# Kernel tuning notes

Measured on AMD Instinct MI355X. Metric: run time of the kernel, lower is better.

Reference implementation:

```python
import jax, jax.numpy as jnp
import numpy as np

N_NODES = 100000
N_EDGES = 3200000
D_IN = 128
D_OUT = 128


def setup_inputs() -> dict:
    key = jax.random.key(0)
    k1, k2, k3, k4, k5, k6 = jax.random.split(key, 6)
    x = jax.random.normal(k1, (N_NODES, D_IN), dtype=jnp.float32)
    stdv = 1.0 / np.sqrt(D_OUT)
    weight = jax.random.normal(k2, (D_IN, D_OUT), dtype=jnp.float32) * stdv
    bias = jax.random.normal(k3, (D_OUT,), dtype=jnp.float32) * stdv
    edge_row = jax.random.randint(k4, (N_EDGES,), 0, N_NODES, dtype=jnp.int32)
    edge_col = jax.random.randint(k5, (N_EDGES,), 0, N_NODES, dtype=jnp.int32)
    edge_vals = jax.random.uniform(k6, (N_EDGES,), dtype=jnp.float32)
    return {"x": x, "weight": weight, "bias": bias,
            "edge_row": edge_row, "edge_col": edge_col, "edge_vals": edge_vals}


def reference(x, weight, bias, edge_row, edge_col, edge_vals):
    # support = input @ W   (dense GEMM, [N, D_out])
    support = x @ weight
    # spmm = adj @ support  with adj in COO form: out[r] += v * support[c]
    messages = edge_vals[:, None] * support[edge_col]  # [E, D_out]
    agg = jax.ops.segment_sum(messages, edge_row, num_segments=N_NODES)
    return agg + bias
```

## Files before the change

kernel.cpp:

```cpp
#include <hip/hip_runtime.h>

#define D 128
#define GEMM_ROWS 32
#define NB_MAX 1600
#define T_TILES 256

__device__ __forceinline__ unsigned bf16_rne(float f) {
    const unsigned u = __float_as_uint(f);
    return (u + 0x7FFFu + ((u >> 16) & 1u)) >> 16;
}
__device__ __forceinline__ float bf_lo(unsigned u) { return __uint_as_float(u << 16); }
__device__ __forceinline__ float bf_hi(unsigned u) { return __uint_as_float(u & 0xFFFF0000u); }

__global__ __launch_bounds__(256) void gcn_gemm(const float* __restrict__ x,
                                                const float* __restrict__ w,
                                                unsigned* __restrict__ support,
                                                int n_nodes) {
    __shared__ float w_lds[D][D];
    __shared__ float x_lds[GEMM_ROWS][D];
    const int t = threadIdx.x;

    {
        const float4* w4 = (const float4*)w;
        float4* wl = (float4*)&w_lds[0][0];
#pragma unroll
        for (int i = 0; i < 16; ++i) wl[t + 256 * i] = w4[t + 256 * i];
    }
    const long row_base = (long)blockIdx.x * GEMM_ROWS;
    {
        const float4* x4 = (const float4*)(x + row_base * D);
        float4* xl = (float4*)&x_lds[0][0];
#pragma unroll
        for (int i = 0; i < 4; ++i) xl[t + 256 * i] = x4[t + 256 * i];
    }
    __syncthreads();

    const int c = t & 31;
    const int rg = t >> 5;

    float4 acc[4];
#pragma unroll
    for (int j = 0; j < 4; ++j) acc[j] = make_float4(0.f, 0.f, 0.f, 0.f);

#pragma unroll 4
    for (int k = 0; k < D; ++k) {
        const float4 wv = ((const float4*)&w_lds[k][0])[c];
#pragma unroll
        for (int j = 0; j < 4; ++j) {
            const float xv = x_lds[rg * 4 + j][k];
            acc[j].x += xv * wv.x;
            acc[j].y += xv * wv.y;
            acc[j].z += xv * wv.z;
            acc[j].w += xv * wv.w;
        }
    }

#pragma unroll
    for (int j = 0; j < 4; ++j) {
        const long r = row_base + rg * 4 + j;
        uint2 pk;
        pk.x = bf16_rne(acc[j].x) | (bf16_rne(acc[j].y) << 16);
        pk.y = bf16_rne(acc[j].z) | (bf16_rne(acc[j].w) << 16);
        ((uint2*)support)[r * 32 + c] = pk;
    }
}

__global__ __launch_bounds__(1024) void gcn_tile_hist(const int* __restrict__ erow,
                                                      int* __restrict__ M,
                                                      int n_edges, int tile_sz, int nb) {
    __shared__ int h[NB_MAX];
    const int t = threadIdx.x;
    for (int i = t; i < nb; i += 1024) h[i] = 0;
    __syncthreads();
    const int beg = blockIdx.x * tile_sz;
    const int end = min(beg + tile_sz, n_edges);
    for (int e = beg + t; e < end; e += 1024)
        atomicAdd(&h[erow[e] >> 6], 1);
    __syncthreads();
    int* Mrow = M + (long)blockIdx.x * nb;
    for (int i = t; i < nb; i += 1024) Mrow[i] = h[i];
}

__global__ __launch_bounds__(256) void gcn_tile_offsets(int* __restrict__ M,
                                                        int* __restrict__ totals,
                                                        int nb) {
    const int cb = blockIdx.x * 256 + threadIdx.x;
    if (cb >= nb) return;
    int running = 0;
#pragma unroll 8
    for (int tt = 0; tt < T_TILES; ++tt) {
        int* p = M + (long)tt * nb + cb;
        const int c = *p;
        *p = running;
        running += c;
    }
    totals[cb] = running;
}

__global__ __launch_bounds__(1024) void gcn_scan_base(const int* __restrict__ totals,
                                                      int* __restrict__ base, int nb) {
    __shared__ int sdata[1024];
    const int t = threadIdx.x;
    const int chunk = (nb + 1023) >> 10;
    const int beg = min(t * chunk, nb);
    const int end = min(beg + chunk, nb);

    int sum = 0;
    for (int i = beg; i < end; ++i) sum += totals[i];
    sdata[t] = sum;
    __syncthreads();
    for (int off = 1; off < 1024; off <<= 1) {
        const int v = (t >= off) ? sdata[t - off] : 0;
        __syncthreads();
        sdata[t] += v;
        __syncthreads();
    }
    int running = sdata[t] - sum;
    if (t == 1023) base[nb] = sdata[1023];
    for (int i = beg; i < end; ++i) {
        const int c = totals[i];
        base[i] = running;
        running += c;
    }
}

__global__ __launch_bounds__(1024) void gcn_split(const int* __restrict__ erow,
                                                  const int* __restrict__ ecol,
                                                  const float* __restrict__ eval,
                                                  const int* __restrict__ M,
                                                  const int* __restrict__ base,
                                                  int2* __restrict__ tmp,
                                                  int n_edges, int tile_sz, int nb) {
    __shared__ int off[NB_MAX];
    const int t = threadIdx.x;
    const int* Mrow = M + (long)blockIdx.x * nb;
    for (int i = t; i < nb; i += 1024) off[i] = Mrow[i] + base[i];
    __syncthreads();
    const int beg = blockIdx.x * tile_sz;
    const int end = min(beg + tile_sz, n_edges);
    for (int e = beg + t; e < end; e += 1024) {
        const int r = erow[e];
        const int pos = atomicAdd(&off[r >> 6], 1);
        const unsigned key = ((unsigned)(r & 63) << 17) | (unsigned)ecol[e];
        tmp[pos] = make_int2((int)key, __float_as_int(eval[e]));
    }
}

__global__ __launch_bounds__(256) void gcn_bucket_fill(const int2* __restrict__ tmp,
                                                       const int* __restrict__ base,
                                                       int2* __restrict__ packed,
                                                       int* __restrict__ rp,
                                                       int n_nodes) {
    __shared__ int hist[64];
    __shared__ int offs[64];
    const int t = threadIdx.x;
    const int cb = blockIdx.x;
    const int start = base[cb];
    const int stop = base[cb + 1];

    if (t < 64) hist[t] = 0;
    __syncthreads();
    for (int i = start + t; i < stop; i += 256)
        atomicAdd(&hist[(unsigned)tmp[i].x >> 17], 1);
    __syncthreads();
    if (t == 0) {
        int run = 0;
#pragma unroll
        for (int i = 0; i < 64; ++i) { offs[i] = run; run += hist[i]; }
    }
    __syncthreads();
    if (t < 64) {
        const int r = cb * 64 + t;
        if (r < n_nodes) rp[r] = start + offs[t];
    }
    __syncthreads();
    for (int i = start + t; i < stop; i += 256) {
        const int2 ed = tmp[i];
        const int rl = (int)((unsigned)ed.x >> 17);
        const int pos = start + atomicAdd(&offs[rl], 1);
        packed[pos] = make_int2(ed.x & 0x1FFFF, ed.y);
    }
}

__global__ __launch_bounds__(512) void gcn_aggregate(const uint4* __restrict__ support4,
                                                     const int2* __restrict__ packed,
                                                     const int* __restrict__ rp,
                                                     const float* __restrict__ bias,
                                                     float* __restrict__ out,
                                                     int n_nodes, int n_edges) {
    const int t = threadIdx.x;
    const int lane = t & 63;
    const int sub = lane & 15;
    const int g = lane >> 4;
    const int r = blockIdx.x * 8 + (t >> 6);
    if (r >= n_nodes) return;

    const int start = rp[r];
    const int end = (r + 1 < n_nodes) ? rp[r + 1] : n_edges;

    float acc[8];
#pragma unroll
    for (int k = 0; k < 8; ++k) acc[k] = 0.f;

    for (int b = start; b < end; b += 64) {
        const int nn = min(64, end - b);
        int2 ed = make_int2(0, 0);
        if (lane < nn) ed = packed[b + lane];
        const int nbat = (nn + 3) >> 2;
#pragma unroll 2
        for (int i = 0; i < nbat; ++i) {
            const int idx = i * 4 + g;
            const int c = __shfl(ed.x, idx, 64);
            float v = __int_as_float(__shfl(ed.y, idx, 64));
            if (idx >= nn) v = 0.f;
            const uint4 pv = support4[(long)c * 16 + sub];
            acc[0] += v * bf_lo(pv.x);
            acc[1] += v * bf_hi(pv.x);
            acc[2] += v * bf_lo(pv.y);
            acc[3] += v * bf_hi(pv.y);
            acc[4] += v * bf_lo(pv.z);
            acc[5] += v * bf_hi(pv.z);
            acc[6] += v * bf_lo(pv.w);
            acc[7] += v * bf_hi(pv.w);
        }
    }

#pragma unroll
    for (int k = 0; k < 8; ++k) {
        acc[k] += __shfl_xor(acc[k], 16, 64);
        acc[k] += __shfl_xor(acc[k], 32, 64);
    }

    if (g == 0) {
        const float4 b0 = ((const float4*)bias)[sub * 2];
        const float4 b1 = ((const float4*)bias)[sub * 2 + 1];
        float4 o0 = make_float4(acc[0] + b0.x, acc[1] + b0.y, acc[2] + b0.z, acc[3] + b0.w);
        float4 o1 = make_float4(acc[4] + b1.x, acc[5] + b1.y, acc[6] + b1.z, acc[7] + b1.w);
        float4* orow = (float4*)(out + (long)r * D);
        orow[sub * 2] = o0;
        orow[sub * 2 + 1] = o1;
    }
}

extern "C" void kernel_launch(void* const* d_in, const int* in_sizes, int n_in,
                              void* d_out, int out_size, void* d_ws, size_t ws_size,
                              hipStream_t stream) {
    const float* x    = (const float*)d_in[0];
    const float* w    = (const float*)d_in[1];
    const float* bias = (const float*)d_in[2];
    const int* erow   = (const int*)d_in[3];
    const int* ecol   = (const int*)d_in[4];
    const float* eval = (const float*)d_in[5];

    const int n_nodes = in_sizes[0] / D;
    const int n_edges = in_sizes[3];
    const int nb = (n_nodes + 63) >> 6;
    const int tile_sz = (n_edges + T_TILES - 1) / T_TILES;

    char* ws = (char*)d_ws;
    unsigned* support = (unsigned*)ws;
    size_t off = (size_t)n_nodes * (D / 2) * sizeof(unsigned);
    int2* packed = (int2*)(ws + off);
    off += (size_t)n_edges * sizeof(int2);
    int* rp = (int*)(ws + off);

    char* ob = (char*)d_out;
    int2* tmp = (int2*)ob;
    size_t ooff = (size_t)n_edges * sizeof(int2);
    int* M = (int*)(ob + ooff);
    ooff += (size_t)T_TILES * nb * sizeof(int);
    int* totals = (int*)(ob + ooff);
    ooff += (size_t)(nb + 1) * sizeof(int);
    int* base = (int*)(ob + ooff);

    float* out = (float*)d_out;

    gcn_gemm<<<(n_nodes + GEMM_ROWS - 1) / GEMM_ROWS, 256, 0, stream>>>(
        x, w, support, n_nodes);

    gcn_tile_hist<<<T_TILES, 1024, 0, stream>>>(erow, M, n_edges, tile_sz, nb);
    gcn_tile_offsets<<<(nb + 255) / 256, 256, 0, stream>>>(M, totals, nb);
    gcn_scan_base<<<1, 1024, 0, stream>>>(totals, base, nb);
    gcn_split<<<T_TILES, 1024, 0, stream>>>(erow, ecol, eval, M, base, tmp,
                                            n_edges, tile_sz, nb);
    gcn_bucket_fill<<<nb, 256, 0, stream>>>(tmp, base, packed, rp, n_nodes);

    gcn_aggregate<<<(n_nodes + 7) / 8, 512, 0, stream>>>(
        (const uint4*)support, packed, rp, bias, out, n_nodes, n_edges);
}
```

Baseline: 411.4 us.

## Retile GEMM into K-staged register blocks and batch gather loads in aggregate

The GEMM kernel now processes 128-row tiles in four K-slices of 32. Each thread holds an 8x8 register tile, and the x tile in shared memory is stored with a rotation swizzle to avoid bank conflicts. This replaces reloading the whole 64KB weight matrix per 32-row block, cutting LDS footprint and raising arithmetic reuse. The aggregate kernel now issues up to eight independent support-row gathers before accumulating, to expose more memory-level parallelism, and adds an occupancy hint. The cost is higher register pressure in both kernels.

```diff
diff --git a/kernel.cpp b/kernel.cpp
--- a/kernel.cpp
+++ b/kernel.cpp
@@ -1,7 +1,6 @@
 #include <hip/hip_runtime.h>
 
 #define D 128
-#define GEMM_ROWS 32
 #define NB_MAX 1600
 #define T_TILES 256
 
@@ -12,56 +11,84 @@
 __device__ __forceinline__ float bf_lo(unsigned u) { return __uint_as_float(u << 16); }
 __device__ __forceinline__ float bf_hi(unsigned u) { return __uint_as_float(u & 0xFFFF0000u); }
 
-__global__ __launch_bounds__(256) void gcn_gemm(const float* __restrict__ x,
-                                                const float* __restrict__ w,
-                                                unsigned* __restrict__ support,
-                                                int n_nodes) {
-    __shared__ float w_lds[D][D];
-    __shared__ float x_lds[GEMM_ROWS][D];
-    const int t = threadIdx.x;
-
-    {
-        const float4* w4 = (const float4*)w;
-        float4* wl = (float4*)&w_lds[0][0];
-#pragma unroll
-        for (int i = 0; i < 16; ++i) wl[t + 256 * i] = w4[t + 256 * i];
-    }
-    const long row_base = (long)blockIdx.x * GEMM_ROWS;
-    {
-        const float4* x4 = (const float4*)(x + row_base * D);
-        float4* xl = (float4*)&x_lds[0][0];
-#pragma unroll
-        for (int i = 0; i < 4; ++i) xl[t + 256 * i] = x4[t + 256 * i];
-    }
-    __syncthreads();
-
-    const int c = t & 31;
-    const int rg = t >> 5;
-
-    float4 acc[4];
-#pragma unroll
-    for (int j = 0; j < 4; ++j) acc[j] = make_float4(0.f, 0.f, 0.f, 0.f);
-
-#pragma unroll 4
-    for (int k = 0; k < D; ++k) {
-        const float4 wv = ((const float4*)&w_lds[k][0])[c];
-#pragma unroll
-        for (int j = 0; j < 4; ++j) {
-            const float xv = x_lds[rg * 4 + j][k];
-            acc[j].x += xv * wv.x;
-            acc[j].y += xv * wv.y;
-            acc[j].z += xv * wv.z;
-            acc[j].w += xv * wv.w;
-        }
-    }
-
-#pragma unroll
-    for (int j = 0; j < 4; ++j) {
-        const long r = row_base + rg * 4 + j;
-        uint2 pk;
-        pk.x = bf16_rne(acc[j].x) | (bf16_rne(acc[j].y) << 16);
-        pk.y = bf16_rne(acc[j].z) | (bf16_rne(acc[j].w) << 16);
-        ((uint2*)support)[r * 32 + c] = pk;
+__global__ __launch_bounds__(256, 4) void gcn_gemm(const float* __restrict__ x,
+                                                   const float* __restrict__ w,
+                                                   unsigned* __restrict__ support,
+                                                   int n_nodes) {
+    __shared__ float xs[128][32];
+    __shared__ float ws[32][128];
+    const int t = threadIdx.x;
+    const int rg = t >> 4;
+    const int cg = t & 15;
+    const long row_base = (long)blockIdx.x * 128;
+
+    float4 acc[8][2];
+#pragma unroll
+    for (int j = 0; j < 8; ++j) {
+        acc[j][0] = make_float4(0.f, 0.f, 0.f, 0.f);
+        acc[j][1] = make_float4(0.f, 0.f, 0.f, 0.f);
+    }
+
+    for (int s = 0; s < 4; ++s) {
+        const int k0 = s * 32;
+        {
+            const float4* w4 = (const float4*)(w + (long)k0 * D);
+            float4* wl = (float4*)&ws[0][0];
+#pragma unroll
+            for (int i = 0; i < 4; ++i) wl[t + 256 * i] = w4[t + 256 * i];
+        }
+        {
+#pragma unroll
+            for (int i = 0; i < 4; ++i) {
+                const int f = t + 256 * i;
+                const int r = f >> 3;
+                const int jj = f & 7;
+                long gr = row_base + r;
+                if (gr >= n_nodes) gr = n_nodes - 1;
+                const float4 v = ((const float4*)(x + gr * D + k0))[jj];
+                const int cs = (jj * 4 + 8 * (r >> 3)) & 31;
+                ((float4*)&xs[r][0])[cs >> 2] = v;
+            }
+        }
+        __syncthreads();
+
+        const int xrot = 8 * rg;
+#pragma unroll 1
+        for (int kk = 0; kk < 32; kk += 4) {
+            float4 wq[4][2];
+#pragma unroll
+            for (int d = 0; d < 4; ++d) {
+                const float4* wr = (const float4*)&ws[kk + d][0];
+                wq[d][0] = wr[cg];
+                wq[d][1] = wr[cg + 16];
+            }
+            const int xi = ((kk + xrot) & 31) >> 2;
+#pragma unroll
+            for (int j = 0; j < 8; ++j) {
+                const float4 xv = ((const float4*)&xs[rg * 8 + j][0])[xi];
+#define FMA4(A, S, W) A.x += S * W.x; A.y += S * W.y; A.z += S * W.z; A.w += S * W.w
+                FMA4(acc[j][0], xv.x, wq[0][0]); FMA4(acc[j][1], xv.x, wq[0][1]);
+                FMA4(acc[j][0], xv.y, wq[1][0]); FMA4(acc[j][1], xv.y, wq[1][1]);
+                FMA4(acc[j][0], xv.z, wq[2][0]); FMA4(acc[j][1], xv.z, wq[2][1]);
+                FMA4(acc[j][0], xv.w, wq[3][0]); FMA4(acc[j][1], xv.w, wq[3][1]);
+#undef FMA4
+            }
+        }
+        __syncthreads();
+    }
+
+#pragma unroll
+    for (int j = 0; j < 8; ++j) {
+        const long r = row_base + rg * 8 + j;
+        if (r < n_nodes) {
+            uint2 p0, p1;
+            p0.x = bf16_rne(acc[j][0].x) | (bf16_rne(acc[j][0].y) << 16);
+            p0.y = bf16_rne(acc[j][0].z) | (bf16_rne(acc[j][0].w) << 16);
+            p1.x = bf16_rne(acc[j][1].x) | (bf16_rne(acc[j][1].y) << 16);
+            p1.y = bf16_rne(acc[j][1].z) | (bf16_rne(acc[j][1].w) << 16);
+            ((uint2*)support)[r * 32 + cg] = p0;
+            ((uint2*)support)[r * 32 + 16 + cg] = p1;
+        }
     }
 }
 
@@ -182,12 +209,12 @@
     }
 }
 
-__global__ __launch_bounds__(512) void gcn_aggregate(const uint4* __restrict__ support4,
-                                                     const int2* __restrict__ packed,
-                                                     const int* __restrict__ rp,
-                                                     const float* __restrict__ bias,
-                                                     float* __restrict__ out,
-                                                     int n_nodes, int n_edges) {
+__global__ __launch_bounds__(512, 5) void gcn_aggregate(const uint4* __restrict__ support4,
+                                                        const int2* __restrict__ packed,
+                                                        const int* __restrict__ rp,
+                                                        const float* __restrict__ bias,
+                                                        float* __restrict__ out,
+                                                        int n_nodes, int n_edges) {
     const int t = threadIdx.x;
     const int lane = t & 63;
     const int sub = lane & 15;
@@ -207,21 +234,34 @@
         int2 ed = make_int2(0, 0);
         if (lane < nn) ed = packed[b + lane];
         const int nbat = (nn + 3) >> 2;
-#pragma unroll 2
-        for (int i = 0; i < nbat; ++i) {
-            const int idx = i * 4 + g;
-            const int c = __shfl(ed.x, idx, 64);
-            float v = __int_as_float(__shfl(ed.y, idx, 64));
-            if (idx >= nn) v = 0.f;
-            const uint4 pv = support4[(long)c * 16 + sub];
-            acc[0] += v * bf_lo(pv.x);
-            acc[1] += v * bf_hi(pv.x);
-            acc[2] += v * bf_lo(pv.y);
-            acc[3] += v * bf_hi(pv.y);
-            acc[4] += v * bf_lo(pv.z);
-            acc[5] += v * bf_hi(pv.z);
-            acc[6] += v * bf_lo(pv.w);
-            acc[7] += v * bf_hi(pv.w);
+        for (int i0 = 0; i0 < nbat; i0 += 8) {
+            const int nb8 = min(8, nbat - i0);
+            uint4 pv[8];
+            float vv[8];
+#pragma unroll
+            for (int i = 0; i < 8; ++i) {
+                if (i < nb8) {
+                    const int idx = (i0 + i) * 4 + g;
+                    const int c = __shfl(ed.x, idx, 64);
+                    float v = __int_as_float(__shfl(ed.y, idx, 64));
+                    if (idx >= nn) v = 0.f;
+                    vv[i] = v;
+                    pv[i] = support4[(long)c * 16 + sub];
+                }
+            }
+#pragma unroll
+            for (int i = 0; i < 8; ++i) {
+                if (i < nb8) {
+                    acc[0] += vv[i] * bf_lo(pv[i].x);
+                    acc[1] += vv[i] * bf_hi(pv[i].x);
+                    acc[2] += vv[i] * bf_lo(pv[i].y);
+                    acc[3] += vv[i] * bf_hi(pv[i].y);
+                    acc[4] += vv[i] * bf_lo(pv[i].z);
+                    acc[5] += vv[i] * bf_hi(pv[i].z);
+                    acc[6] += vv[i] * bf_lo(pv[i].w);
+                    acc[7] += vv[i] * bf_hi(pv[i].w);
+                }
+            }
         }
     }
 
@@ -275,8 +315,7 @@
 
     float* out = (float*)d_out;
 
-    gcn_gemm<<<(n_nodes + GEMM_ROWS - 1) / GEMM_ROWS, 256, 0, stream>>>(
-        x, w, support, n_nodes);
+    gcn_gemm<<<(n_nodes + 127) / 128, 256, 0, stream>>>(x, w, support, n_nodes);
 
     gcn_tile_hist<<<T_TILES, 1024, 0, stream>>>(erow, M, n_edges, tile_sz, nb);
     gcn_tile_offsets<<<(nb + 255) / 256, 256, 0, stream>>>(M, totals, nb);
```

Result: slower. 450.6 us (+9.5%).
